# Kernel optimization log

Hardware: AMD Instinct MI355X
Metric: run time of the kernel (lower is better)

The kernel has to match this reference:

```python
import jax, jax.numpy as jnp
import numpy as np

K_TOP = 2
NUM_HEADS = 8
NOISE_EPS = 0.01
GATE_EPS = 1e-9
LOSS_COEF = 0.01


def _xavier(key, shape):
    fan_in, fan_out = shape[-2], shape[-1]
    lim = float(np.sqrt(6.0 / (fan_in + fan_out)))
    return jax.random.uniform(key, shape, jnp.float32, -lim, lim)


def setup_inputs():
    key = jax.random.key(0)
    ks = jax.random.split(key, 12)
    B, S, D, E = 32, 512, 512, 8
    return {
        "q": jax.random.normal(ks[0], (B, S, D), jnp.float32),
        "k": jax.random.normal(ks[1], (B, S, D), jnp.float32),
        "v": jax.random.normal(ks[2], (B, S, D), jnp.float32),
        "mask": jnp.ones((1, 1, S, S), jnp.int32),
        "w_gate": _xavier(ks[3], (D, E)),
        "w_noise": _xavier(ks[4], (D, E)),
        "Wq": _xavier(ks[5], (E, D, D)),
        "bq": jnp.zeros((E, D), jnp.float32),
        "Wk": _xavier(ks[6], (E, D, D)),
        "bk": jnp.zeros((E, D), jnp.float32),
        "Wv": _xavier(ks[7], (E, D, D)),
        "bv": jnp.zeros((E, D), jnp.float32),
        "Wo": _xavier(ks[8], (E, D, D)),
        "bo": jnp.zeros((E, D), jnp.float32),
    }


def _cv_squared(x):
    # torch .var() is unbiased (ddof=1)
    return jnp.var(x, ddof=1) / (jnp.mean(x) ** 2 + 1e-10)


def _moe_attention(q, k, v, mask, w_gate, w_noise, Wq, bq, Wk, bk, Wv, bv, Wo, bo):
    B, S, D = q.shape
    E = w_gate.shape[1]
    H = NUM_HEADS
    dh = D // H

    # x[x != x] = 0 (in-place nan scrub of q, used for gating AND as query)
    qc = jnp.where(jnp.isnan(q), jnp.zeros((), q.dtype), q)

    # noisy top-k gating; the python loop sum_i x[:,i,:] @ W == x.sum(1) @ W
    xs = qc.sum(axis=1)                                  # [B, D]
    clean_logits = xs @ w_gate                           # [B, E]
    raw_noise = xs @ w_noise
    noise_std = jax.nn.softplus(raw_noise) + NOISE_EPS   # train=True
    noise = jax.random.normal(jax.random.key(42), clean_logits.shape, clean_logits.dtype)
    noisy_logits = clean_logits + noise * noise_std

    top_logits, top_idx = jax.lax.top_k(noisy_logits, K_TOP + 1)  # [B, k+1]
    tk_logits = top_logits[:, :K_TOP]
    tk_idx = top_idx[:, :K_TOP]                          # [B, k]
    tk_gates = jax.nn.softmax(tk_logits, axis=1) + GATE_EPS
    gates = jnp.zeros((B, E), clean_logits.dtype).at[jnp.arange(B)[:, None], tk_idx].set(tk_gates)

    # load via prob-in-top-k (noisy_gating and k < num_experts)
    thr_in = top_logits[:, K_TOP][:, None]
    thr_out = top_logits[:, K_TOP - 1][:, None]
    is_in = noisy_logits > thr_in
    cdf = jax.scipy.stats.norm.cdf
    prob = jnp.where(is_in, cdf((clean_logits - thr_in) / noise_std),
                     cdf((clean_logits - thr_out) / noise_std))
    load = prob.sum(axis=0)
    importance = gates.sum(axis=0)
    loss = (_cv_squared(importance) + _cv_squared(load)) * LOSS_COEF

    # sparse dispatch == per (batch, slot) run the selected expert's MHA.
    # Gather expert weights per selected slot: [B, k, D, D].
    def proj(x, W, b):
        return jnp.einsum('bsd,bjdf->bjsf', x, W[tk_idx]) + b[tk_idx][:, :, None, :]

    Q = proj(qc, Wq, bq).reshape(B, K_TOP, S, H, dh)
    Kx = proj(k, Wk, bk).reshape(B, K_TOP, S, H, dh)
    V = proj(v, Wv, bv).reshape(B, K_TOP, S, H, dh)

    scale = jnp.asarray(1.0 / np.sqrt(dh), q.dtype)
    scores = jnp.einsum('bjqhd,bjkhd->bjhqk', Q, Kx) * scale   # [B,k,H,S,S]
    m = mask[:, None]                                          # [1,1,1,S,S]
    scores = jnp.where(m == 0, jnp.asarray(-1e9, scores.dtype), scores)
    attn = jax.nn.softmax(scores, axis=-1)
    ctx = jnp.einsum('bjhqk,bjkhd->bjqhd', attn, V).reshape(B, K_TOP, S, D)
    out_e = jnp.einsum('bjsd,bjdf->bjsf', ctx, Wo[tk_idx]) + bo[tk_idx][:, :, None, :]

    # combine: sum_j gate * exp(out), clamp zeros to eps, log
    combined = jnp.einsum('bj,bjsd->bsd', tk_gates, jnp.exp(out_e))
    eps = jnp.asarray(np.finfo(np.float64).eps, combined.dtype)
    combined = jnp.where(combined == 0, eps, combined)
    return jnp.log(combined), loss


def reference(q, k, v, mask, w_gate, w_noise, Wq, bq, Wk, bk, Wv, bv, Wo, bo):
    return _moe_attention(q, k, v, mask, w_gate, w_noise, Wq, bq, Wk, bk, Wv, bv, Wo, bo)
```

## Files before the change

kernel.cpp:

```cpp
#include <hip/hip_runtime.h>
#include <math.h>

typedef unsigned int u32;
typedef unsigned long long u64;
typedef unsigned short u16t;

#define SD   512
#define EE   8
#define DH   64
#define SDSQ (512*512)
#define LDSW 72

#define QSC  0.18033688011112042f
#define LOG2E 1.4426950408889634f
#define LN2   0.6931471805599453f

typedef __attribute__((ext_vector_type(8))) short bfrag8;
typedef __attribute__((ext_vector_type(4))) float f32x4;
typedef __attribute__((ext_vector_type(8))) unsigned short u16x8;

typedef const __attribute__((address_space(1))) void gas_void;
typedef __attribute__((address_space(3))) void las_void;

#define MFMA_B16(a,b,c) __builtin_amdgcn_mfma_f32_16x16x32_bf16((a),(b),(c),0,0,0)

__device__ __forceinline__ u32 rotl32(u32 x, int r){ return (x<<r)|(x>>(32-r)); }

__device__ __forceinline__ u16t bf_hi(float a){
  u32 x; __builtin_memcpy(&x,&a,4);
  u32 r = x + 0x7fffu + ((x>>16)&1u);
  return (u16t)(r>>16);
}
__device__ __forceinline__ float bf_f(u16t h){
  u32 x = ((u32)h)<<16; float f; __builtin_memcpy(&f,&x,4); return f;
}
__device__ __forceinline__ void split2(float a, u16t& h, u16t& l){
  h = bf_hi(a);
  l = bf_hi(a - bf_f(h));
}

__device__ __forceinline__ void gload16(const u16t* g, u16t* l){
  __builtin_amdgcn_global_load_lds((gas_void*)g, (las_void*)l, 16, 0, 0);
}

__device__ __forceinline__ void threefry_0_42(u32 x0, u32 x1, u32& o0, u32& o1){
  const u32 k0=0u, k1=42u;
  const u32 ks2 = k0 ^ k1 ^ 0x1BD11BDAu;
  const int R0[4]={13,15,26,6}, R1[4]={17,29,16,24};
  x0 += k0; x1 += k1;
  #pragma unroll
  for(int r=0;r<4;r++){ x0+=x1; x1=rotl32(x1,R0[r]); x1^=x0; }
  x0+=k1; x1+=ks2+1u;
  #pragma unroll
  for(int r=0;r<4;r++){ x0+=x1; x1=rotl32(x1,R1[r]); x1^=x0; }
  x0+=ks2; x1+=k0+2u;
  #pragma unroll
  for(int r=0;r<4;r++){ x0+=x1; x1=rotl32(x1,R0[r]); x1^=x0; }
  x0+=k0; x1+=k1+3u;
  #pragma unroll
  for(int r=0;r<4;r++){ x0+=x1; x1=rotl32(x1,R1[r]); x1^=x0; }
  x0+=k1; x1+=ks2+4u;
  #pragma unroll
  for(int r=0;r<4;r++){ x0+=x1; x1=rotl32(x1,R0[r]); x1^=x0; }
  x0+=ks2; x1+=k0+5u;
  o0 = x0; o1 = x1;
}

__device__ double erfinv64(double x){
  double w = -log((1.0 - x) * (1.0 + x));
  double p;
  if (w < 5.0){
    w = w - 2.5;
    p = 2.81022636e-08;
    p = 3.43273939e-07 + p*w;
    p = -3.5233877e-06 + p*w;
    p = -4.39150654e-06 + p*w;
    p = 0.00021858087  + p*w;
    p = -0.00125372503 + p*w;
    p = -0.00417768164 + p*w;
    p = 0.246640727    + p*w;
    p = 1.50140941     + p*w;
  } else {
    w = sqrt(w) - 3.0;
    p = -0.000200214257;
    p = 0.000100950558 + p*w;
    p = 0.00134934322  + p*w;
    p = -0.00367342844 + p*w;
    p = 0.00573950773  + p*w;
    p = -0.0076224613  + p*w;
    p = 0.00943887047  + p*w;
    p = 1.00167406     + p*w;
    p = 2.83297682     + p*w;
  }
  double r = p * x;
  #pragma unroll
  for (int it=0; it<2; ++it){
    double e = erf(r) - x;
    r -= e / (1.1283791670955126 * exp(-r*r));
  }
  return r;
}

__device__ double jax_noise_part32(int i){
  u32 o0, o1;
  threefry_0_42(0u, (u32)i, o0, o1);
  u32 bits = o0 ^ o1;
  u32 fb = (bits >> 9) | 0x3f800000u;
  float f; __builtin_memcpy(&f, &fb, 4);
  f -= 1.0f;
  u32 lob = 0xBF7FFFFFu;
  float lo; __builtin_memcpy(&lo, &lob, 4);
  float t = f * 2.0f;
  float u = t + lo;
  u = fmaxf(u, lo);
  return 1.4142135623730951 * erfinv64((double)u);
}

__global__ __launch_bounds__(256) void k_cvt_x(
  const float* __restrict__ src, u16t* __restrict__ dh, u16t* __restrict__ dl, int clean)
{
  const int n4 = 32*SDSQ/4;
  int i = blockIdx.x*256 + threadIdx.x;
  if (i >= n4) return;
  float4 r = ((const float4*)src)[i];
  float a[4] = {r.x, r.y, r.z, r.w};
  if (clean){
    #pragma unroll
    for (int u=0;u<4;u++) if (isnan(a[u])) a[u] = 0.f;
  }
  u16t h[4], l[4];
  #pragma unroll
  for (int u=0;u<4;u++) split2(a[u], h[u], l[u]);
  ((ushort4*)dh)[i] = make_ushort4(h[0],h[1],h[2],h[3]);
  ((ushort4*)dl)[i] = make_ushort4(l[0],l[1],l[2],l[3]);
}

__global__ __launch_bounds__(256) void k_cvt_w(
  const float* __restrict__ W, u16t* __restrict__ th, u16t* __restrict__ tl)
{
  __shared__ u16t Th[64*LDSW], Tl[64*LDSW];
  int e = blockIdx.z;
  int k0 = blockIdx.y*64, f0 = blockIdx.x*64;
  int tid = threadIdx.x;
  int r = tid>>2, c4 = (tid&3)*16;
  const float* Wp = W + (size_t)e*SDSQ + (size_t)(k0+r)*SD + f0 + c4;
  #pragma unroll
  for (int i=0;i<4;i++){
    float4 rv = *(const float4*)(Wp + 4*i);
    float a[4]={rv.x,rv.y,rv.z,rv.w};
    #pragma unroll
    for (int u=0;u<4;u++){
      u16t h,l; split2(a[u],h,l);
      Th[(c4+4*i+u)*LDSW + r] = h;
      Tl[(c4+4*i+u)*LDSW + r] = l;
    }
  }
  __syncthreads();
  u16t* dh = th + (size_t)e*SDSQ + (size_t)(f0+r)*SD + k0 + c4;
  u16t* dl = tl + (size_t)e*SDSQ + (size_t)(f0+r)*SD + k0 + c4;
  *(u16x8*)dh     = *(const u16x8*)&Th[r*LDSW + c4];
  *(u16x8*)(dh+8) = *(const u16x8*)&Th[r*LDSW + c4 + 8];
  *(u16x8*)dl     = *(const u16x8*)&Tl[r*LDSW + c4];
  *(u16x8*)(dl+8) = *(const u16x8*)&Tl[r*LDSW + c4 + 8];
}

__global__ void k_xs(const float* __restrict__ q, double* __restrict__ xs){
  int b = blockIdx.x, d = blockIdx.y*128 + threadIdx.x;
  const float* p = q + (size_t)b*SDSQ + d;
  double acc = 0.0;
  for (int s=0; s<SD; ++s){
    float f = p[(size_t)s*SD];
    if (!isnan(f)) acc += (double)f;
  }
  xs[b*SD + d] = acc;
}

__global__ __launch_bounds__(256) void k_gate(
    const double* __restrict__ xs, const float* __restrict__ wg,
    const float* __restrict__ wn, int* __restrict__ tk_idx,
    float* __restrict__ tk_gates, float* __restrict__ out_loss)
{
  __shared__ double cl_s[256], sd_s[256], nz_s[256], pr_s[256];
  __shared__ double thrI_s[32], thrO_s[32], g0_s[32], g1_s[32];
  __shared__ int i0_s[32], i1_s[32];
  int tid = threadIdx.x;
  int b = tid >> 3, e = tid & 7;
  double c=0.0, n=0.0;
  const double* xr = xs + b*SD;
  for (int d=0; d<SD; ++d){
    double x = xr[d];
    c += x * (double)wg[d*EE + e];
    n += x * (double)wn[d*EE + e];
  }
  double sp = fmax(n, 0.0) + log1p(exp(-fabs(n)));
  double sdv = sp + 0.01;
  double nz = c + jax_noise_part32(tid) * sdv;
  cl_s[tid]=c; sd_s[tid]=sdv; nz_s[tid]=nz;
  __syncthreads();
  if (tid < 32){
    int bb = tid;
    double v0=-INFINITY,v1=-INFINITY,v2=-INFINITY; int i0=0,i1=0;
    for (int ee=0; ee<8; ++ee){
      double vv = nz_s[bb*8+ee];
      if (vv > v0){ v2=v1; v1=v0;i1=i0; v0=vv;i0=ee; }
      else if (vv > v1){ v2=v1; v1=vv;i1=ee; }
      else if (vv > v2){ v2=vv; }
    }
    double e1 = exp(v1 - v0);
    double s = 1.0 + e1;
    double g0 = 1.0/s + 1e-9, g1 = e1/s + 1e-9;
    tk_idx[bb*2+0]=i0; tk_idx[bb*2+1]=i1;
    tk_gates[bb*2+0]=(float)g0; tk_gates[bb*2+1]=(float)g1;
    i0_s[bb]=i0; i1_s[bb]=i1; g0_s[bb]=g0; g1_s[bb]=g1;
    thrI_s[bb]=v2; thrO_s[bb]=v1;
  }
  __syncthreads();
  {
    double thrI = thrI_s[b], thrO = thrO_s[b];
    bool isin = nz_s[tid] > thrI;
    double t = (cl_s[tid] - (isin ? thrI : thrO)) / sd_s[tid];
    pr_s[tid] = 0.5 * (1.0 + erf(t * 0.7071067811865476));
  }
  __syncthreads();
  if (tid == 0){
    double imp[8], ld[8];
    for (int i=0;i<8;i++){ imp[i]=0.0; ld[i]=0.0; }
    for (int bb=0; bb<32; ++bb){
      imp[i0_s[bb]] += g0_s[bb];
      imp[i1_s[bb]] += g1_s[bb];
    }
    for (int i=0;i<256;i++) ld[i&7] += pr_s[i];
    double loss = 0.0;
    for (int a=0;a<2;a++){
      double* arr = a ? ld : imp;
      double mu=0.0; for(int i=0;i<8;i++) mu += arr[i]; mu *= 0.125;
      double var=0.0; for(int i=0;i<8;i++){ double dd=arr[i]-mu; var += dd*dd; }
      var *= (1.0/7.0);
      loss += var / (mu*mu + 1e-10);
    }
    loss *= 0.01;
    out_loss[0] = (float)loss;
  }
}

__global__ __launch_bounds__(256) void k_proj(
  const u16t* __restrict__ qh, const u16t* __restrict__ ql,
  const u16t* __restrict__ kh, const u16t* __restrict__ kl,
  const u16t* __restrict__ vh, const u16t* __restrict__ vl,
  const u16t* __restrict__ wqh, const u16t* __restrict__ wql,
  const u16t* __restrict__ wkh, const u16t* __restrict__ wkl,
  const u16t* __restrict__ wvh, const u16t* __restrict__ wvl,
  const float* __restrict__ bq, const float* __restrict__ bk, const float* __restrict__ bv,
  const int* __restrict__ tk_idx, int pair0,
  u16t* __restrict__ Qh, u16t* __restrict__ Ql,
  u16t* __restrict__ Kh, u16t* __restrict__ Kl,
  u16t* __restrict__ Vth, u16t* __restrict__ Vtl)
{
  __shared__ __align__(16) u16t SM[4*128*64];
  int Nb = gridDim.x*gridDim.y*gridDim.z;
  int flat = blockIdx.x + gridDim.x*(blockIdx.y + gridDim.y*blockIdx.z);
  int nf = (flat & 7)*(Nb>>3) + (flat>>3);
  int bxx = nf & 3, byy = (nf>>2) & 3, z = nf >> 4;
  int lp = z/3, m = z - lp*3;
  int gp = pair0 + lp;
  int b = gp >> 1;
  int e = tk_idx[gp] & 7;
  const u16t *Xh, *Xl, *Wh, *Wl; const float* bias; u16t *Yh, *Yl;
  if (m==0){ Xh=qh; Xl=ql; Wh=wqh; Wl=wql; bias=bq; Yh=Qh;  Yl=Ql;  }
  else if (m==1){ Xh=kh; Xl=kl; Wh=wkh; Wl=wkl; bias=bk; Yh=Kh;  Yl=Kl;  }
  else { Xh=vh; Xl=vl; Wh=wvh; Wl=wvl; bias=bv; Yh=Vth; Yl=Vtl; }
  bool tr = (m==2);
  float ysc = (m==0) ? QSC : 1.0f;
  Xh += (size_t)b*SDSQ; Xl += (size_t)b*SDSQ;
  Wh += (size_t)e*SDSQ; Wl += (size_t)e*SDSQ;
  bias += e*SD;
  Yh += (size_t)lp*SDSQ; Yl += (size_t)lp*SDSQ;

  int tid = threadIdx.x, w = tid>>6, lane = tid&63;
  int q16 = lane&15, quad = lane>>4;
  int wm = w>>1, wnn = w&1;
  int s0 = byy*128, f0 = bxx*128;
  int row8 = lane>>3, cc = lane&7;
  int soff = (cc ^ row8)*8;
  int sw = q16 & 7;
  int aH_off = tr ? 16384 : 0;
  int bH_off = tr ? 0 : 16384;

  f32x4 acc[4][4];
  #pragma unroll
  for (int i=0;i<4;i++)
    #pragma unroll
    for (int j=0;j<4;j++) acc[i][j] = (f32x4){0.f,0.f,0.f,0.f};

  for (int k0=0;k0<SD;k0+=64){
    #pragma unroll
    for (int t=0;t<4;t++){
      int br = w*32 + t*8;
      int gr = br + row8;
      size_t ga  = (size_t)(s0+gr)*SD + k0 + soff;
      size_t gbo = (size_t)(f0+gr)*SD + k0 + soff;
      gload16(Xh + ga,  &SM[0     + br*64]);
      gload16(Xl + ga,  &SM[8192  + br*64]);
      gload16(Wh + gbo, &SM[16384 + br*64]);
      gload16(Wl + gbo, &SM[24576 + br*64]);
    }
    __syncthreads();
    #pragma unroll
    for (int kk=0;kk<2;kk++){
      int ch = kk*4 + quad;
      int co = (ch ^ sw)*8;
      bfrag8 fAH[4], fAL[4], fBH[4], fBL[4];
      #pragma unroll
      for (int i=0;i<4;i++){
        int ra = wm*64  + i*16 + q16;
        int rb = wnn*64 + i*16 + q16;
        fAH[i] = *(const bfrag8*)&SM[aH_off        + ra*64 + co];
        fAL[i] = *(const bfrag8*)&SM[aH_off + 8192 + ra*64 + co];
        fBH[i] = *(const bfrag8*)&SM[bH_off        + rb*64 + co];
        fBL[i] = *(const bfrag8*)&SM[bH_off + 8192 + rb*64 + co];
      }
      #pragma unroll
      for (int i=0;i<4;i++)
        #pragma unroll
        for (int j=0;j<4;j++){
          acc[i][j] = MFMA_B16(fAH[i], fBH[j], acc[i][j]);
          acc[i][j] = MFMA_B16(fAH[i], fBL[j], acc[i][j]);
          acc[i][j] = MFMA_B16(fAL[i], fBH[j], acc[i][j]);
        }
    }
    __syncthreads();
  }
  if (!tr){
    #pragma unroll
    for (int i=0;i<4;i++){
      #pragma unroll
      for (int j=0;j<4;j++){
        int f = f0 + wnn*64 + j*16 + q16;
        float bb = bias[f];
        #pragma unroll
        for (int rr=0;rr<4;rr++){
          int s = s0 + wm*64 + i*16 + quad*4 + rr;
          u16t hh, ll; split2((acc[i][j][rr] + bb)*ysc, hh, ll);
          size_t o = (size_t)s*SD + f;
          Yh[o] = hh; Yl[o] = ll;
        }
      }
    }
  } else {
    #pragma unroll
    for (int i=0;i<4;i++){
      #pragma unroll
      for (int rr=0;rr<4;rr++){
        int fr = f0 + wm*64 + i*16 + quad*4 + rr;
        float bb = bias[fr];
        #pragma unroll
        for (int j=0;j<4;j++){
          int scol = s0 + wnn*64 + j*16 + q16;
          u16t hh, ll; split2(acc[i][j][rr] + bb, hh, ll);
          size_t o = (size_t)fr*SD + scol;
          Yh[o] = hh; Yl[o] = ll;
        }
      }
    }
  }
}

__global__ __launch_bounds__(256, 4) void k_attn(
  const u16t* __restrict__ Qh, const u16t* __restrict__ Ql,
  const u16t* __restrict__ Kh, const u16t* __restrict__ Kl,
  const u16t* __restrict__ Vth, const u16t* __restrict__ Vtl,
  u16t* __restrict__ Ch, u16t* __restrict__ Cl)
{
  __shared__ __align__(16) u16t SM[20480];
  int tid = threadIdx.x;
  int w = tid>>6, lane = tid&63, q16 = lane&15, quad = lane>>4;
  int Nb = gridDim.x*gridDim.y*gridDim.z;
  int flat = blockIdx.x + gridDim.x*(blockIdx.y + gridDim.y*blockIdx.z);
  int nf = (flat & 7)*(Nb>>3) + (flat>>3);
  int qt = nf & 7, h = (nf>>3) & 7, lp = nf >> 6;
  int s0 = qt*64;
  const size_t base  = (size_t)lp*SDSQ + h*DH;
  const size_t vbase = (size_t)lp*SDSQ + (size_t)h*DH*SD;
  int row8 = lane>>3, cc = lane&7;
  int soff = (cc ^ row8)*8;
  int sw = q16 & 7;

  bfrag8 qH[2], qL[2];
  {
    const u16t* qp  = Qh + base + (size_t)(s0 + w*16 + q16)*SD + quad*8;
    const u16t* qp2 = Ql + base + (size_t)(s0 + w*16 + q16)*SD + quad*8;
    qH[0] = *(const bfrag8*)(qp);
    qH[1] = *(const bfrag8*)(qp + 32);
    qL[0] = *(const bfrag8*)(qp2);
    qL[1] = *(const bfrag8*)(qp2 + 32);
  }

  float m_row[4], l_row[4];
  f32x4 ctx[4];
  #pragma unroll
  for (int rr=0;rr<4;rr++){ m_row[rr]=-INFINITY; l_row[rr]=0.f; }
  #pragma unroll
  for (int nt=0;nt<4;nt++) ctx[nt] = (f32x4){0.f,0.f,0.f,0.f};

  for (int kt=0; kt<8; ++kt){
    #pragma unroll
    for (int t=0;t<2;t++){
      int br = w*16 + t*8;
      int gr = br + row8;
      size_t gk = base + (size_t)(kt*64+gr)*SD + soff;
      gload16(Kh + gk, &SM[0    + br*64]);
      gload16(Kl + gk, &SM[4096 + br*64]);
      size_t gv = vbase + (size_t)gr*SD + kt*64 + soff;
      gload16(Vth + gv, &SM[8192  + br*64]);
      gload16(Vtl + gv, &SM[12288 + br*64]);
    }
    __syncthreads();

    f32x4 sc[4];
    #pragma unroll
    for (int nt=0;nt<4;nt++) sc[nt] = (f32x4){0.f,0.f,0.f,0.f};
    #pragma unroll
    for (int kk=0;kk<2;kk++){
      int co = ((kk*4+quad) ^ sw)*8;
      #pragma unroll
      for (int nt=0;nt<4;nt++){
        bfrag8 bH = *(const bfrag8*)&SM[0    + (nt*16+q16)*64 + co];
        bfrag8 bL = *(const bfrag8*)&SM[4096 + (nt*16+q16)*64 + co];
        sc[nt] = MFMA_B16(qH[kk],bH,sc[nt]);
        sc[nt] = MFMA_B16(qH[kk],bL,sc[nt]);
        sc[nt] = MFMA_B16(qL[kk],bH,sc[nt]);
      }
    }

    float mx4[4];
    bool grow = false;
    #pragma unroll
    for (int rr=0;rr<4;rr++){
      float mx = sc[0][rr];
      #pragma unroll
      for (int nt=1;nt<4;nt++) mx = fmaxf(mx, sc[nt][rr]);
      mx = fmaxf(mx, __shfl_xor(mx, 1));
      mx = fmaxf(mx, __shfl_xor(mx, 2));
      mx = fmaxf(mx, __shfl_xor(mx, 4));
      mx = fmaxf(mx, __shfl_xor(mx, 8));
      mx4[rr] = mx;
      grow = grow || (mx > m_row[rr] + 8.f);
    }
    if (__any(grow ? 1 : 0)){
      #pragma unroll
      for (int rr=0;rr<4;rr++){
        float nm = fmaxf(m_row[rr], mx4[rr]);
        float al = exp2f(m_row[rr] - nm);
        m_row[rr] = nm;
        l_row[rr] *= al;
        #pragma unroll
        for (int nt=0;nt<4;nt++) ctx[nt][rr] *= al;
      }
    }
    #pragma unroll
    for (int rr=0;rr<4;rr++){
      float S = 0.f;
      #pragma unroll
      for (int nt=0;nt<4;nt++){
        float p = exp2f(sc[nt][rr] - m_row[rr]);
        sc[nt][rr] = p;
        S += p;
      }
      S += __shfl_xor(S, 1);
      S += __shfl_xor(S, 2);
      S += __shfl_xor(S, 4);
      S += __shfl_xor(S, 8);
      l_row[rr] += S;
    }
    #pragma unroll
    for (int nt=0;nt<4;nt++){
      int c = nt*2 + (q16>>3);
      #pragma unroll
      for (int rr=0;rr<4;rr++){
        int prow = quad*4 + rr;
        SM[16384 + (w*16+prow)*64 + ((c ^ (prow&7))*8) + (q16&7)] = bf_hi(sc[nt][rr]);
      }
    }

    #pragma unroll
    for (int kk2=0;kk2<2;kk2++){
      int co2 = ((kk2*4+quad) ^ sw)*8;
      bfrag8 aP = *(const bfrag8*)&SM[16384 + (w*16+q16)*64 + co2];
      #pragma unroll
      for (int nt=0;nt<4;nt++){
        bfrag8 vH = *(const bfrag8*)&SM[8192  + (nt*16+q16)*64 + co2];
        bfrag8 vL = *(const bfrag8*)&SM[12288 + (nt*16+q16)*64 + co2];
        ctx[nt] = MFMA_B16(aP,vH,ctx[nt]);
        ctx[nt] = MFMA_B16(aP,vL,ctx[nt]);
      }
    }
    __syncthreads();
  }
  #pragma unroll
  for (int rr=0;rr<4;rr++){
    float inv = 1.f / l_row[rr];
    #pragma unroll
    for (int nt=0;nt<4;nt++){
      int s = s0 + w*16 + quad*4 + rr;
      u16t hh, ll; split2(ctx[nt][rr]*inv, hh, ll);
      size_t o = base + (size_t)s*SD + nt*16 + q16;
      Ch[o] = hh; Cl[o] = ll;
    }
  }
}

__global__ __launch_bounds__(256) void k_out(
  const u16t* __restrict__ Ch, const u16t* __restrict__ Cl,
  const u16t* __restrict__ Wth, const u16t* __restrict__ Wtl,
  const float* __restrict__ bo, const int* __restrict__ tk_idx,
  const float* __restrict__ tk_gates, int pair0, float* __restrict__ out)
{
  __shared__ __align__(16) u16t Ah[64*64], Al[64*64];
  __shared__ __align__(16) u16t Bh[64*64], Bl[64*64];
  int Nb = gridDim.x*gridDim.y*gridDim.z;
  int flat = blockIdx.x + gridDim.x*(blockIdx.y + gridDim.y*blockIdx.z);
  int nf = (flat & 7)*(Nb>>3) + (flat>>3);
  int bxx = nf & 7, byy = (nf>>3) & 7, lb = nf >> 6;
  int gb = (pair0 >> 1) + lb;
  int tid = threadIdx.x;
  int w = tid>>6, lane = tid&63, q16 = lane&15, quad = lane>>4;
  int s0 = byy*64, f0 = bxx*64;
  int row8 = lane>>3, cc = lane&7;
  int soff = (cc ^ row8)*8;
  int sw = q16 & 7;

  f32x4 acc2[2][4];
  #pragma unroll
  for (int j=0;j<2;j++)
    #pragma unroll
    for (int nt=0;nt<4;nt++) acc2[j][nt] = (f32x4){0.f,0.f,0.f,0.f};

  for (int j=0;j<2;++j){
    int e = tk_idx[pair0 + lb*2 + j] & 7;
    const u16t* AH = Ch + (size_t)(lb*2+j)*SDSQ;
    const u16t* AL = Cl + (size_t)(lb*2+j)*SDSQ;
    const u16t* WH = Wth + (size_t)e*SDSQ;
    const u16t* WL = Wtl + (size_t)e*SDSQ;
    for (int k0=0;k0<SD;k0+=64){
      #pragma unroll
      for (int t=0;t<2;t++){
        int br = w*16 + t*8, gr = br + row8;
        size_t ga  = (size_t)(s0+gr)*SD + k0 + soff;
        size_t gbo = (size_t)(f0+gr)*SD + k0 + soff;
        gload16(AH + ga,  &Ah[br*64]);
        gload16(AL + ga,  &Al[br*64]);
        gload16(WH + gbo, &Bh[br*64]);
        gload16(WL + gbo, &Bl[br*64]);
      }
      __syncthreads();
      #pragma unroll
      for (int kk=0;kk<2;kk++){
        int co = ((kk*4+quad) ^ sw)*8;
        bfrag8 aH = *(const bfrag8*)&Ah[(w*16+q16)*64 + co];
        bfrag8 aL = *(const bfrag8*)&Al[(w*16+q16)*64 + co];
        #pragma unroll
        for (int nt=0;nt<4;nt++){
          bfrag8 bH = *(const bfrag8*)&Bh[(nt*16+q16)*64 + co];
          bfrag8 bL = *(const bfrag8*)&Bl[(nt*16+q16)*64 + co];
          acc2[j][nt] = MFMA_B16(aH,bH,acc2[j][nt]);
          acc2[j][nt] = MFMA_B16(aH,bL,acc2[j][nt]);
          acc2[j][nt] = MFMA_B16(aL,bH,acc2[j][nt]);
        }
      }
      __syncthreads();
    }
  }
  int e0 = tk_idx[pair0 + lb*2 + 0] & 7, e1 = tk_idx[pair0 + lb*2 + 1] & 7;
  float g0 = tk_gates[pair0 + lb*2 + 0], g1 = tk_gates[pair0 + lb*2 + 1];
  #pragma unroll
  for (int nt=0;nt<4;nt++){
    #pragma unroll
    for (int rr=0;rr<4;rr++){
      int s = s0 + w*16 + quad*4 + rr;
      int f = f0 + nt*16 + q16;
      float o0 = acc2[0][nt][rr] + bo[e0*SD+f];
      float o1 = acc2[1][nt][rr] + bo[e1*SD+f];
      float cmb = g0*exp2f(o0*LOG2E) + g1*exp2f(o1*LOG2E);
      if (cmb == 0.f) cmb = 2.2204460492503131e-16f;
      out[(size_t)gb*SDSQ + (size_t)s*SD + f] = log2f(cmb)*LN2;
    }
  }
}

extern "C" void kernel_launch(void* const* d_in, const int* in_sizes, int n_in,
                              void* d_out, int out_size, void* d_ws, size_t ws_size,
                              hipStream_t stream)
{
  const float* q  = (const float*)d_in[0];
  const float* k  = (const float*)d_in[1];
  const float* v  = (const float*)d_in[2];
  const float* wg = (const float*)d_in[4];
  const float* wn = (const float*)d_in[5];
  const float* Wq = (const float*)d_in[6];
  const float* bq = (const float*)d_in[7];
  const float* Wk = (const float*)d_in[8];
  const float* bk = (const float*)d_in[9];
  const float* Wv = (const float*)d_in[10];
  const float* bv = (const float*)d_in[11];
  const float* Wo = (const float*)d_in[12];
  const float* bo = (const float*)d_in[13];
  float* out = (float*)d_out;

  char* ws = (char*)d_ws;
  double* xs      = (double*)(ws + 0);
  int*   tk_idx   = (int*)  (ws + 131072);
  float* tk_gates = (float*)(ws + 131072 + 256);

  const size_t header = (size_t)1 << 20;
  const size_t XSB = (size_t)32 * SDSQ * 2;
  const size_t WSB = (size_t)8  * SDSQ * 2;
  u16t* qch = (u16t*)(ws + header + 0*XSB);
  u16t* qcl = (u16t*)(ws + header + 1*XSB);
  u16t* kh_ = (u16t*)(ws + header + 2*XSB);
  u16t* kl_ = (u16t*)(ws + header + 3*XSB);
  u16t* vh_ = (u16t*)(ws + header + 4*XSB);
  u16t* vl_ = (u16t*)(ws + header + 5*XSB);
  char* wbase = ws + header + 6*XSB;
  u16t* wqh = (u16t*)(wbase + 0*WSB);
  u16t* wql = (u16t*)(wbase + 1*WSB);
  u16t* wkh = (u16t*)(wbase + 2*WSB);
  u16t* wkl = (u16t*)(wbase + 3*WSB);
  u16t* wvh = (u16t*)(wbase + 4*WSB);
  u16t* wvl = (u16t*)(wbase + 5*WSB);
  u16t* woh = (u16t*)(wbase + 6*WSB);
  u16t* wol = (u16t*)(wbase + 7*WSB);
  char* bufbase = wbase + 8*WSB;

  const size_t slab = (size_t)SDSQ * 2;
  size_t used = (size_t)(bufbase - ws);
  size_t avail = (ws_size > used) ? (ws_size - used) : 0;
  int CH = (int)(avail / (6 * slab));
  CH &= ~1;
  if (CH > 64) CH = 64;
  if (CH < 2)  CH = 2;

  k_cvt_x<<<dim3(8192), dim3(256), 0, stream>>>(q, qch, qcl, 1);
  k_cvt_x<<<dim3(8192), dim3(256), 0, stream>>>(k, kh_, kl_, 0);
  k_cvt_x<<<dim3(8192), dim3(256), 0, stream>>>(v, vh_, vl_, 0);
  k_cvt_w<<<dim3(8,8,8), dim3(256), 0, stream>>>(Wq, wqh, wql);
  k_cvt_w<<<dim3(8,8,8), dim3(256), 0, stream>>>(Wk, wkh, wkl);
  k_cvt_w<<<dim3(8,8,8), dim3(256), 0, stream>>>(Wv, wvh, wvl);
  k_cvt_w<<<dim3(8,8,8), dim3(256), 0, stream>>>(Wo, woh, wol);

  k_xs  <<<dim3(32,4), dim3(128), 0, stream>>>(q, xs);
  k_gate<<<dim3(1), dim3(256), 0, stream>>>(xs, wg, wn, tk_idx, tk_gates,
                                            out + (size_t)out_size - 1);

  for (int pair0 = 0; pair0 < 64; pair0 += CH){
    int cur = (64 - pair0 < CH) ? (64 - pair0) : CH;
    u16t* Qh  = (u16t*)bufbase;
    u16t* Ql  = Qh  + (size_t)CH * SDSQ;
    u16t* Kh  = Ql  + (size_t)CH * SDSQ;
    u16t* Kl  = Kh  + (size_t)CH * SDSQ;
    u16t* Vth = Kl  + (size_t)CH * SDSQ;
    u16t* Vtl = Vth + (size_t)CH * SDSQ;
    u16t* Ch = Qh;
    u16t* Cl = Ql;

    k_proj<<<dim3(4,4,cur*3), dim3(256), 0, stream>>>(
        qch,qcl, kh_,kl_, vh_,vl_, wqh,wql, wkh,wkl, wvh,wvl,
        bq,bk,bv, tk_idx, pair0, Qh,Ql, Kh,Kl, Vth,Vtl);
    k_attn<<<dim3(8,8,cur), dim3(256), 0, stream>>>(Qh,Ql, Kh,Kl, Vth,Vtl, Ch,Cl);
    k_out <<<dim3(8,8,cur/2), dim3(256), 0, stream>>>(Ch,Cl, woh,wol, bo, tk_idx, tk_gates,
                                                      pair0, out);
  }
}
```

Baseline: 697.2 us.

## Enlarge k_out tile to 128x128 with 2x2 warp layout for more reuse

The output projection kernel moves from 64x64 tiles to 128x128 tiles, with each of the four waves computing a 64x64 sub-tile using 4x4 MFMA fragments. Each loaded LDS fragment now feeds more MFMAs, which cuts global and LDS traffic per FLOP. The cost is many more accumulator registers (128 floats for two experts), lower occupancy, and fewer blocks in the grid, which may underfill the GPU.

```diff
diff --git a/kernel.cpp b/kernel.cpp
--- a/kernel.cpp
+++ b/kernel.cpp
@@ -515,26 +515,29 @@
   const float* __restrict__ bo, const int* __restrict__ tk_idx,
   const float* __restrict__ tk_gates, int pair0, float* __restrict__ out)
 {
-  __shared__ __align__(16) u16t Ah[64*64], Al[64*64];
-  __shared__ __align__(16) u16t Bh[64*64], Bl[64*64];
+  __shared__ __align__(16) u16t SM[4*128*64];
   int Nb = gridDim.x*gridDim.y*gridDim.z;
   int flat = blockIdx.x + gridDim.x*(blockIdx.y + gridDim.y*blockIdx.z);
   int nf = (flat & 7)*(Nb>>3) + (flat>>3);
-  int bxx = nf & 7, byy = (nf>>3) & 7, lb = nf >> 6;
+  int bxx = nf & 3, byy = (nf>>2) & 3, lb = nf >> 4;
   int gb = (pair0 >> 1) + lb;
-  int tid = threadIdx.x;
-  int w = tid>>6, lane = tid&63, q16 = lane&15, quad = lane>>4;
-  int s0 = byy*64, f0 = bxx*64;
+  int tid = threadIdx.x, w = tid>>6, lane = tid&63;
+  int q16 = lane&15, quad = lane>>4;
+  int wm = w>>1, wnn = w&1;
+  int s0 = byy*128, f0 = bxx*128;
   int row8 = lane>>3, cc = lane&7;
   int soff = (cc ^ row8)*8;
   int sw = q16 & 7;
 
-  f32x4 acc2[2][4];
+  f32x4 acc2[2][4][4];
   #pragma unroll
   for (int j=0;j<2;j++)
     #pragma unroll
-    for (int nt=0;nt<4;nt++) acc2[j][nt] = (f32x4){0.f,0.f,0.f,0.f};
-
+    for (int i=0;i<4;i++)
+      #pragma unroll
+      for (int j4=0;j4<4;j4++) acc2[j][i][j4] = (f32x4){0.f,0.f,0.f,0.f};
+
+  #pragma unroll 1
   for (int j=0;j<2;++j){
     int e = tk_idx[pair0 + lb*2 + j] & 7;
     const u16t* AH = Ch + (size_t)(lb*2+j)*SDSQ;
@@ -543,29 +546,39 @@
     const u16t* WL = Wtl + (size_t)e*SDSQ;
     for (int k0=0;k0<SD;k0+=64){
       #pragma unroll
-      for (int t=0;t<2;t++){
-        int br = w*16 + t*8, gr = br + row8;
+      for (int t=0;t<4;t++){
+        int br = w*32 + t*8;
+        int gr = br + row8;
         size_t ga  = (size_t)(s0+gr)*SD + k0 + soff;
         size_t gbo = (size_t)(f0+gr)*SD + k0 + soff;
-        gload16(AH + ga,  &Ah[br*64]);
-        gload16(AL + ga,  &Al[br*64]);
-        gload16(WH + gbo, &Bh[br*64]);
-        gload16(WL + gbo, &Bl[br*64]);
+        gload16(AH + ga,  &SM[0     + br*64]);
+        gload16(AL + ga,  &SM[8192  + br*64]);
+        gload16(WH + gbo, &SM[16384 + br*64]);
+        gload16(WL + gbo, &SM[24576 + br*64]);
       }
       __syncthreads();
       #pragma unroll
       for (int kk=0;kk<2;kk++){
-        int co = ((kk*4+quad) ^ sw)*8;
-        bfrag8 aH = *(const bfrag8*)&Ah[(w*16+q16)*64 + co];
-        bfrag8 aL = *(const bfrag8*)&Al[(w*16+q16)*64 + co];
+        int ch = kk*4 + quad;
+        int co = (ch ^ sw)*8;
+        bfrag8 fAH[4], fAL[4], fBH[4], fBL[4];
         #pragma unroll
-        for (int nt=0;nt<4;nt++){
-          bfrag8 bH = *(const bfrag8*)&Bh[(nt*16+q16)*64 + co];
-          bfrag8 bL = *(const bfrag8*)&Bl[(nt*16+q16)*64 + co];
-          acc2[j][nt] = MFMA_B16(aH,bH,acc2[j][nt]);
-          acc2[j][nt] = MFMA_B16(aH,bL,acc2[j][nt]);
-          acc2[j][nt] = MFMA_B16(aL,bH,acc2[j][nt]);
+        for (int i=0;i<4;i++){
+          int ra = wm*64  + i*16 + q16;
+          int rb = wnn*64 + i*16 + q16;
+          fAH[i] = *(const bfrag8*)&SM[0     + ra*64 + co];
+          fAL[i] = *(const bfrag8*)&SM[8192  + ra*64 + co];
+          fBH[i] = *(const bfrag8*)&SM[16384 + rb*64 + co];
+          fBL[i] = *(const bfrag8*)&SM[24576 + rb*64 + co];
         }
+        #pragma unroll
+        for (int i=0;i<4;i++)
+          #pragma unroll
+          for (int j4=0;j4<4;j4++){
+            acc2[j][i][j4] = MFMA_B16(fAH[i], fBH[j4], acc2[j][i][j4]);
+            acc2[j][i][j4] = MFMA_B16(fAH[i], fBL[j4], acc2[j][i][j4]);
+            acc2[j][i][j4] = MFMA_B16(fAL[i], fBH[j4], acc2[j][i][j4]);
+          }
       }
       __syncthreads();
     }
@@ -573,16 +586,20 @@
   int e0 = tk_idx[pair0 + lb*2 + 0] & 7, e1 = tk_idx[pair0 + lb*2 + 1] & 7;
   float g0 = tk_gates[pair0 + lb*2 + 0], g1 = tk_gates[pair0 + lb*2 + 1];
   #pragma unroll
-  for (int nt=0;nt<4;nt++){
-    #pragma unroll
-    for (int rr=0;rr<4;rr++){
-      int s = s0 + w*16 + quad*4 + rr;
-      int f = f0 + nt*16 + q16;
-      float o0 = acc2[0][nt][rr] + bo[e0*SD+f];
-      float o1 = acc2[1][nt][rr] + bo[e1*SD+f];
-      float cmb = g0*exp2f(o0*LOG2E) + g1*exp2f(o1*LOG2E);
-      if (cmb == 0.f) cmb = 2.2204460492503131e-16f;
-      out[(size_t)gb*SDSQ + (size_t)s*SD + f] = log2f(cmb)*LN2;
+  for (int i=0;i<4;i++){
+    #pragma unroll
+    for (int j4=0;j4<4;j4++){
+      int f = f0 + wnn*64 + j4*16 + q16;
+      float b0 = bo[e0*SD+f], b1 = bo[e1*SD+f];
+      #pragma unroll
+      for (int rr=0;rr<4;rr++){
+        int s = s0 + wm*64 + i*16 + quad*4 + rr;
+        float o0 = acc2[0][i][j4][rr] + b0;
+        float o1 = acc2[1][i][j4][rr] + b1;
+        float cmb = g0*exp2f(o0*LOG2E) + g1*exp2f(o1*LOG2E);
+        if (cmb == 0.f) cmb = 2.2204460492503131e-16f;
+        out[(size_t)gb*SDSQ + (size_t)s*SD + f] = log2f(cmb)*LN2;
+      }
     }
   }
 }
@@ -666,7 +683,7 @@
         qch,qcl, kh_,kl_, vh_,vl_, wqh,wql, wkh,wkl, wvh,wvl,
         bq,bk,bv, tk_idx, pair0, Qh,Ql, Kh,Kl, Vth,Vtl);
     k_attn<<<dim3(8,8,cur), dim3(256), 0, stream>>>(Qh,Ql, Kh,Kl, Vth,Vtl, Ch,Cl);
-    k_out <<<dim3(8,8,cur/2), dim3(256), 0, stream>>>(Ch,Cl, woh,wol, bo, tk_idx, tk_gates,
+    k_out <<<dim3(4,4,cur/2), dim3(256), 0, stream>>>(Ch,Cl, woh,wol, bo, tk_idx, tk_gates,
                                                       pair0, out);
   }
 }
```

Result: slower. 1.003 ms (+43.9%).
